# Kernel tuning notes

Measured on AMD Instinct MI355X. Metric: run time of the kernel, lower is better.

## Reference

```python
import jax, jax.numpy as jnp
import numpy as np

B, S, E = 2, 2048, 1024
H = 16
D = E // H  # 64
SCALE = D ** -0.5


def setup_inputs() -> dict:
    key = jax.random.key(0)
    ks = jax.random.split(key, 9)
    w = lambda k: jax.random.normal(k, (E, E), dtype=jnp.float32) * 0.02
    b = lambda k: jax.random.normal(k, (E,), dtype=jnp.float32) * 0.02
    return {
        "hidden_states": jax.random.normal(ks[0], (B, S, E), dtype=jnp.float32),
        "q_w": w(ks[1]), "q_b": b(ks[2]),
        "k_w": w(ks[3]), "k_b": b(ks[4]),
        "v_w": w(ks[5]), "v_b": b(ks[6]),
        "o_w": w(ks[7]), "o_b": b(ks[8]),
    }


def reference(hidden_states, q_w, q_b, k_w, k_b, v_w, v_b, o_w, o_b):
    dtype = hidden_states.dtype
    # torch Linear: y = x @ W^T + b
    q = hidden_states @ q_w.T + q_b
    k = hidden_states @ k_w.T + k_b
    v = hidden_states @ v_w.T + v_b
    # [B,S,E] -> [B*H, S, D]
    split = lambda t: t.reshape(B, S, H, D).transpose(0, 2, 1, 3).reshape(B * H, S, D)
    q, k, v = split(q), split(k), split(v)
    # upcast_attention: fp32 QK^T, scaled (baddbmm with beta=0, no mask)
    scores = SCALE * jnp.einsum("bqd,bkd->bqk", q.astype(jnp.float32), k.astype(jnp.float32))
    # upcast_softmax: fp32 softmax over last dim (transpose_qk=False), cast back
    probs = jax.nn.softmax(scores, axis=-1).astype(dtype)
    # PV bmm, merge heads, out_proj (dropout p=0.0 -> identity)
    out = jnp.einsum("bqk,bkd->bqd", probs, v)
    out = out.reshape(B, H, S, D).transpose(0, 2, 1, 3).reshape(B, S, E)
    return out @ o_w.T + o_b
```

## Files before the change

kernel.cpp:

```cpp
#include <hip/hip_runtime.h>

typedef __bf16 bf16x8 __attribute__((ext_vector_type(8)));
typedef __bf16 bf16x4 __attribute__((ext_vector_type(4)));
typedef float  f32x4  __attribute__((ext_vector_type(4)));
typedef float  f32x16 __attribute__((ext_vector_type(16)));
typedef unsigned int u32x4 __attribute__((ext_vector_type(4)));

#define CS 0.18033688011112042f

__device__ __forceinline__ float fast_exp2(float x) {
    return __builtin_amdgcn_exp2f(x);
}

__device__ __forceinline__ f32x4 MFMA(bf16x8 a, bf16x8 b, f32x4 c) {
    return __builtin_amdgcn_mfma_f32_16x16x32_bf16(a, b, c, 0, 0, 0);
}
__device__ __forceinline__ f32x16 MFMA32(bf16x8 a, bf16x8 b, f32x16 c) {
    return __builtin_amdgcn_mfma_f32_32x32x16_bf16(a, b, c, 0, 0, 0);
}

__device__ __forceinline__ unsigned pk2(float a, float b) {
    union { __bf16 h[2]; unsigned u; } x;
    x.h[0] = (__bf16)a; x.h[1] = (__bf16)b;
    return x.u;
}

__device__ __forceinline__ void swap32(unsigned &a, unsigned &b) {
    asm volatile("v_permlane32_swap_b32 %0, %1" : "+v"(a), "+v"(b));
}

__global__ __launch_bounds__(256) void cvt5_kernel(
    const float* __restrict__ s0, const float* __restrict__ s1,
    const float* __restrict__ s2, const float* __restrict__ s3,
    const float* __restrict__ s4,
    __bf16* __restrict__ d0, __bf16* __restrict__ d1, __bf16* __restrict__ d2,
    __bf16* __restrict__ d3, __bf16* __restrict__ d4)
{
    int blk = blockIdx.x;
    const float* src; __bf16* dst; int base;
    if (blk < 4096)      { src = s0; dst = d0; base = blk; }
    else if (blk < 5120) { src = s1; dst = d1; base = blk - 4096; }
    else if (blk < 6144) { src = s2; dst = d2; base = blk - 5120; }
    else if (blk < 7168) { src = s3; dst = d3; base = blk - 6144; }
    else                 { src = s4; dst = d4; base = blk - 7168; }
    int i = base * 1024 + threadIdx.x * 4;
    float4 v = *(const float4*)(src + i);
    bf16x4 o;
    o[0] = (__bf16)v.x; o[1] = (__bf16)v.y; o[2] = (__bf16)v.z; o[3] = (__bf16)v.w;
    *(bf16x4*)(dst + i) = o;
}

template <typename OutT, int BN>
__device__ __forceinline__ void gemm_core(const __bf16* __restrict__ A,
                                          const __bf16* __restrict__ W,
                                          const float* __restrict__ bias,
                                          OutT* __restrict__ C,
                                          int m0, int n0, bool vtrans, float oscale)
{
    constexpr int NJ = BN / 32;
    __shared__ __bf16 As[128 * 64];
    __shared__ __bf16 Bs[BN * 64];

    const int tid  = threadIdx.x;
    const int lane = tid & 63;
    const int w    = tid >> 6;
    const int wm   = w & 1;
    const int wn   = w >> 1;
    const int s    = lane & 15;
    const int q    = lane >> 4;

    f32x4 acc[4][NJ];
#pragma unroll
    for (int i = 0; i < 4; i++)
#pragma unroll
        for (int j = 0; j < NJ; j++)
#pragma unroll
            for (int r = 0; r < 4; r++) acc[i][j][r] = 0.0f;

    bf16x8 apre[4], bpre[NJ];
#pragma unroll
    for (int t = 0; t < 4; t++) {
        int c = tid + 256 * t, row = c >> 3, cc = c & 7;
        apre[t] = *(const bf16x8*)(A + (size_t)(m0 + row) * 1024 + cc * 8);
    }
#pragma unroll
    for (int t = 0; t < NJ; t++) {
        int c = tid + 256 * t, row = c >> 3, cc = c & 7;
        bpre[t] = *(const bf16x8*)(W + (size_t)(n0 + row) * 1024 + cc * 8);
    }

    for (int k0 = 0; k0 < 1024; k0 += 64) {
        __syncthreads();
#pragma unroll
        for (int t = 0; t < 4; t++) {
            int c = tid + 256 * t, row = c >> 3, cc = c & 7;
            *(bf16x8*)&As[row * 64 + ((cc ^ (row & 7)) << 3)] = apre[t];
        }
#pragma unroll
        for (int t = 0; t < NJ; t++) {
            int c = tid + 256 * t, row = c >> 3, cc = c & 7;
            *(bf16x8*)&Bs[row * 64 + ((cc ^ (row & 7)) << 3)] = bpre[t];
        }
        __syncthreads();

        if (k0 < 1024 - 64) {
            int kn = k0 + 64;
#pragma unroll
            for (int t = 0; t < 4; t++) {
                int c = tid + 256 * t, row = c >> 3, cc = c & 7;
                apre[t] = *(const bf16x8*)(A + (size_t)(m0 + row) * 1024 + kn + cc * 8);
            }
#pragma unroll
            for (int t = 0; t < NJ; t++) {
                int c = tid + 256 * t, row = c >> 3, cc = c & 7;
                bpre[t] = *(const bf16x8*)(W + (size_t)(n0 + row) * 1024 + kn + cc * 8);
            }
        }

#pragma unroll
        for (int kk = 0; kk < 2; kk++) {
            bf16x8 af[4], bf[NJ];
#pragma unroll
            for (int i = 0; i < 4; i++) {
                int row = wm * 64 + i * 16 + s;
                int idx = row * 64 + ((((kk << 2) + q) ^ (row & 7)) << 3);
                af[i] = *(const bf16x8*)&As[idx];
            }
#pragma unroll
            for (int j = 0; j < NJ; j++) {
                int row = wn * (BN / 2) + j * 16 + s;
                int idx = row * 64 + ((((kk << 2) + q) ^ (row & 7)) << 3);
                bf[j] = *(const bf16x8*)&Bs[idx];
            }
#pragma unroll
            for (int i = 0; i < 4; i++)
#pragma unroll
                for (int j = 0; j < NJ; j++)
                    acc[i][j] = MFMA(af[i], bf[j], acc[i][j]);
        }
    }

    if (vtrans) {
        __bf16* Vt = (__bf16*)C;
#pragma unroll
        for (int j = 0; j < NJ; j++) {
            int col = n0 + wn * (BN / 2) + j * 16 + s;
            int h   = col >> 6;
            int d   = col & 63;
            float bv = bias[col];
#pragma unroll
            for (int i = 0; i < 4; i++) {
                int rowb = m0 + wm * 64 + i * 16 + q * 4;
                int b    = rowb >> 11;
                int srow = rowb & 2047;
                bf16x4 pk;
#pragma unroll
                for (int r = 0; r < 4; r++) pk[r] = (__bf16)(acc[i][j][r] + bv);
                *(bf16x4*)&Vt[(size_t)((b * 16 + h) * 64 + d) * 2048 + srow] = pk;
            }
        }
    } else {
#pragma unroll
        for (int j = 0; j < NJ; j++) {
            int col = n0 + wn * (BN / 2) + j * 16 + s;
            float bv = bias[col];
#pragma unroll
            for (int i = 0; i < 4; i++) {
                int rowb = m0 + wm * 64 + i * 16 + q * 4;
#pragma unroll
                for (int r = 0; r < 4; r++) {
                    C[(size_t)(rowb + r) * 1024 + col] = (OutT)((acc[i][j][r] + bv) * oscale);
                }
            }
        }
    }
}

__global__ __launch_bounds__(256) void gemm_qkv_kernel(
    const __bf16* __restrict__ X,
    const __bf16* __restrict__ Wq, const float* __restrict__ bq,
    const __bf16* __restrict__ Wk, const float* __restrict__ bk,
    const __bf16* __restrict__ Wv, const float* __restrict__ bv,
    __bf16* __restrict__ Q, __bf16* __restrict__ K, __bf16* __restrict__ Vt)
{
    int mt   = blockIdx.x & 31;
    int ntot = blockIdx.x >> 5;
    int which = ntot >> 3;
    const __bf16* W    = (which == 0) ? Wq : (which == 1) ? Wk : Wv;
    const float*  bias = (which == 0) ? bq : (which == 1) ? bk : bv;
    __bf16*       Out  = (which == 0) ? Q  : (which == 1) ? K  : Vt;
    float oscale = (which == 0) ? CS : 1.0f;
    gemm_core<__bf16, 128>(X, W, bias, Out, mt * 128, (ntot & 7) * 128, which == 2, oscale);
}

__global__ __launch_bounds__(256) void gemm_o_kernel(
    const __bf16* __restrict__ Ain, const __bf16* __restrict__ Wo,
    const float* __restrict__ bo, float* __restrict__ Out)
{
    int mt = blockIdx.x & 31;
    int nt = blockIdx.x >> 5;
    gemm_core<float, 64>(Ain, Wo, bo, Out, mt * 128, nt * 64, false, 1.0f);
}

__global__ __launch_bounds__(512, 4) void attn_kernel(
    const __bf16* __restrict__ Q, const __bf16* __restrict__ K,
    const __bf16* __restrict__ Vt, __bf16* __restrict__ O)
{
    __shared__ __bf16 smem[2][2][2][64 * 64];

    const int bh = blockIdx.x >> 4;
    const int qt = blockIdx.x & 15;
    const int b  = bh >> 4;
    const int h  = bh & 15;

    const int tid  = threadIdx.x;
    const int lane = tid & 63;
    const int w    = tid >> 6;
    const int g    = w >> 2;
    const int ws   = w & 3;
    const int lt   = tid & 255;
    const int qc   = lane & 31;
    const int hi   = lane >> 5;

    bf16x8 bq[4];
    {
        const int qrow = qt * 128 + ws * 32 + qc;
        const __bf16* qp = Q + (size_t)(b * 2048 + qrow) * 1024 + h * 64 + hi * 8;
#pragma unroll
        for (int kd = 0; kd < 4; kd++)
            bq[kd] = *(const bf16x8*)(qp + kd * 16);
    }

    f32x16 acc[2];
#pragma unroll
    for (int nb = 0; nb < 2; nb++)
#pragma unroll
        for (int r = 0; r < 16; r++) acc[nb][r] = 0.0f;
    float lst = 0.0f;

    const __bf16* Kbase = K  + (size_t)(b * 2048 + g * 1024) * 1024 + h * 64;
    const __bf16* Vbase = Vt + (size_t)bh * 64 * 2048 + g * 1024;

    bf16x8 kpre[2], vpre[2];
#pragma unroll
    for (int t = 0; t < 2; t++) {
        int c = lt + 256 * t;
        int krow = c >> 3, s16 = c & 7;
        kpre[t] = *(const bf16x8*)(Kbase + (size_t)krow * 1024 + s16 * 8);
        vpre[t] = *(const bf16x8*)(Vbase + (size_t)krow * 2048 + s16 * 8);
    }
#pragma unroll
    for (int t = 0; t < 2; t++) {
        int c = lt + 256 * t;
        int krow = c >> 3, s16 = c & 7;
        *(bf16x8*)&smem[g][0][0][krow * 64 + ((s16 ^ (krow & 7)) << 3)] = kpre[t];
        *(bf16x8*)&smem[g][0][1][krow * 64 + ((s16 ^ (krow & 7)) << 3)] = vpre[t];
    }
#pragma unroll
    for (int t = 0; t < 2; t++) {
        int c = lt + 256 * t;
        int krow = c >> 3, s16 = c & 7;
        kpre[t] = *(const bf16x8*)(Kbase + (size_t)(64 + krow) * 1024 + s16 * 8);
        vpre[t] = *(const bf16x8*)(Vbase + (size_t)krow * 2048 + 64 + s16 * 8);
    }
    __syncthreads();

    int cur = 0;
    for (int kc = 0; kc < 16; kc++) {
        {
            __bf16* kwb = smem[g][cur ^ 1][0];
            __bf16* vwb = smem[g][cur ^ 1][1];
#pragma unroll
            for (int t = 0; t < 2; t++) {
                int c = lt + 256 * t;
                int krow = c >> 3, s16 = c & 7;
                *(bf16x8*)&kwb[krow * 64 + ((s16 ^ (krow & 7)) << 3)] = kpre[t];
                *(bf16x8*)&vwb[krow * 64 + ((s16 ^ (krow & 7)) << 3)] = vpre[t];
            }
        }
        {
            int kb2 = ((kc + 2) & 15) * 64;
#pragma unroll
            for (int t = 0; t < 2; t++) {
                int c = lt + 256 * t;
                int krow = c >> 3, s16 = c & 7;
                kpre[t] = *(const bf16x8*)(Kbase + (size_t)(kb2 + krow) * 1024 + s16 * 8);
                vpre[t] = *(const bf16x8*)(Vbase + (size_t)krow * 2048 + kb2 + s16 * 8);
            }
        }

        const __bf16* kbuf = smem[g][cur][0];
        const __bf16* vbuf = smem[g][cur][1];

        f32x16 sc[2];
#pragma unroll
        for (int mb = 0; mb < 2; mb++)
#pragma unroll
            for (int r = 0; r < 16; r++) sc[mb][r] = 0.0f;
#pragma unroll
        for (int mb = 0; mb < 2; mb++) {
            int row = mb * 32 + qc;
            int rsw = row & 7;
#pragma unroll
            for (int kd = 0; kd < 4; kd++) {
                bf16x8 af = *(const bf16x8*)&kbuf[row * 64 + ((((kd << 1) | hi) ^ rsw) << 3)];
                sc[mb] = MFMA32(af, bq[kd], sc[mb]);
            }
        }

#pragma unroll
        for (int mb = 0; mb < 2; mb++) {
            float e[16];
#pragma unroll
            for (int r = 0; r < 16; r++)
                e[r] = fast_exp2(sc[mb][r]);
            float s0 = 0.f, s1 = 0.f, s2 = 0.f, s3 = 0.f;
#pragma unroll
            for (int r = 0; r < 16; r += 4) {
                s0 += e[r]; s1 += e[r + 1]; s2 += e[r + 2]; s3 += e[r + 3];
            }
            lst += (s0 + s1) + (s2 + s3);
#pragma unroll
            for (int bb = 0; bb < 2; bb++) {
                unsigned w0 = pk2(e[8 * bb + 0], e[8 * bb + 1]);
                unsigned w1 = pk2(e[8 * bb + 2], e[8 * bb + 3]);
                unsigned w2 = pk2(e[8 * bb + 4], e[8 * bb + 5]);
                unsigned w3 = pk2(e[8 * bb + 6], e[8 * bb + 7]);
                swap32(w0, w2);
                swap32(w1, w3);
                u32x4 pw; pw[0] = w0; pw[1] = w1; pw[2] = w2; pw[3] = w3;
                bf16x8 pa = __builtin_bit_cast(bf16x8, pw);
                int kslot = ((mb << 1) | bb) << 1;
#pragma unroll
                for (int nb = 0; nb < 2; nb++) {
                    int d = nb * 32 + qc;
                    bf16x8 bv = *(const bf16x8*)&vbuf[d * 64 + (((kslot | hi) ^ (d & 7)) << 3)];
                    acc[nb] = MFMA32(pa, bv, acc[nb]);
                }
            }
        }
        __syncthreads();
        cur ^= 1;
    }

    float* cbuf = (float*)&smem[0][0][0][0];
    if (g == 1) {
        float* p = cbuf + ((size_t)ws * 64 + lane) * 36;
        *(f32x16*)(p)      = acc[0];
        *(f32x16*)(p + 16) = acc[1];
        p[32] = lst;
    }
    __syncthreads();
    if (g == 0) {
        float* p = cbuf + ((size_t)ws * 64 + lane) * 36;
        acc[0] += *(const f32x16*)(p);
        acc[1] += *(const f32x16*)(p + 16);
        lst += p[32];

        float lt2 = lst + __shfl_xor(lst, 32);

        const size_t obase = (size_t)(b * 2048 + qt * 128 + ws * 32) * 1024 + h * 64;
#pragma unroll
        for (int r = 0; r < 16; r++) {
            int row_rel = (r & 3) + 8 * (r >> 2) + 4 * hi;
            float lr = __shfl(lt2, row_rel);
            float inv = 1.0f / lr;
#pragma unroll
            for (int nb = 0; nb < 2; nb++) {
                O[obase + (size_t)row_rel * 1024 + nb * 32 + qc] = (__bf16)(acc[nb][r] * inv);
            }
        }
    }
}

extern "C" void kernel_launch(void* const* d_in, const int* in_sizes, int n_in,
                              void* d_out, int out_size, void* d_ws, size_t ws_size,
                              hipStream_t stream)
{
    const float* hs = (const float*)d_in[0];
    const float* qw = (const float*)d_in[1];
    const float* qb = (const float*)d_in[2];
    const float* kw = (const float*)d_in[3];
    const float* kb = (const float*)d_in[4];
    const float* vw = (const float*)d_in[5];
    const float* vb = (const float*)d_in[6];
    const float* ow = (const float*)d_in[7];
    const float* ob = (const float*)d_in[8];
    float* out = (float*)d_out;

    char* ws = (char*)d_ws;
    const size_t MB = (size_t)1024 * 1024;
    __bf16* Xb  = (__bf16*)(ws);
    __bf16* Wqb = (__bf16*)(ws +  8 * MB);
    __bf16* Wkb = (__bf16*)(ws + 10 * MB);
    __bf16* Wvb = (__bf16*)(ws + 12 * MB);
    __bf16* Wob = (__bf16*)(ws + 14 * MB);
    __bf16* Qb  = (__bf16*)(ws + 16 * MB);
    __bf16* Kb  = (__bf16*)(ws + 24 * MB);
    __bf16* Vtb = (__bf16*)(ws + 32 * MB);
    __bf16* Ab  = (__bf16*)(ws + 40 * MB);

    cvt5_kernel<<<dim3(8192), dim3(256), 0, stream>>>(hs, qw, kw, vw, ow,
                                                      Xb, Wqb, Wkb, Wvb, Wob);

    gemm_qkv_kernel<<<dim3(768), dim3(256), 0, stream>>>(Xb, Wqb, qb, Wkb, kb, Wvb, vb,
                                                         Qb, Kb, Vtb);
    attn_kernel<<<dim3(512), dim3(512), 0, stream>>>(Qb, Kb, Vtb, Ab);
    gemm_o_kernel<<<dim3(512), dim3(256), 0, stream>>>(Ab, Wob, ob, out);
}
```

Measured before the change: 193.6 us.

## Load GEMM tiles via global_load_lds and raise priority around attention MFMAs

The projection GEMM stops staging tiles through registers and instead uses direct global-to-LDS 16-byte loads. The software prefetch and the XOR swizzle are dropped, so the tiles are now stored unswizzled in LDS. In the attention kernel, the MFMA calls are wrapped in s_setprio to favour matrix issue, and the score accumulator is initialised by the first MFMA. The GEMM loses its overlap of the next tile's global loads with compute and may now see LDS bank conflicts, in exchange for lower VGPR use and fewer instructions.

```diff
diff --git a/kernel.cpp b/kernel.cpp
--- a/kernel.cpp
+++ b/kernel.cpp
@@ -10,6 +10,12 @@
 
 __device__ __forceinline__ float fast_exp2(float x) {
     return __builtin_amdgcn_exp2f(x);
+}
+
+__device__ __forceinline__ void gload_lds16(const __bf16* g, __bf16* l) {
+    __builtin_amdgcn_global_load_lds(
+        (const __attribute__((address_space(1))) void*)g,
+        (__attribute__((address_space(3))) void*)l, 16, 0, 0);
 }
 
 __device__ __forceinline__ f32x4 MFMA(bf16x8 a, bf16x8 b, f32x4 c) {
@@ -57,7 +63,8 @@
                                           OutT* __restrict__ C,
                                           int m0, int n0, bool vtrans, float oscale)
 {
-    constexpr int NJ = BN / 32;
+    constexpr int NJ  = BN / 32;
+    constexpr int BCH = BN / 32;
     __shared__ __bf16 As[128 * 64];
     __shared__ __bf16 Bs[BN * 64];
 
@@ -69,6 +76,9 @@
     const int s    = lane & 15;
     const int q    = lane >> 4;
 
+    const int srow = lane >> 3;
+    const int scol = lane & 7;
+
     f32x4 acc[4][NJ];
 #pragma unroll
     for (int i = 0; i < 4; i++)
@@ -76,46 +86,24 @@
         for (int j = 0; j < NJ; j++)
 #pragma unroll
             for (int r = 0; r < 4; r++) acc[i][j][r] = 0.0f;
-
-    bf16x8 apre[4], bpre[NJ];
-#pragma unroll
-    for (int t = 0; t < 4; t++) {
-        int c = tid + 256 * t, row = c >> 3, cc = c & 7;
-        apre[t] = *(const bf16x8*)(A + (size_t)(m0 + row) * 1024 + cc * 8);
-    }
-#pragma unroll
-    for (int t = 0; t < NJ; t++) {
-        int c = tid + 256 * t, row = c >> 3, cc = c & 7;
-        bpre[t] = *(const bf16x8*)(W + (size_t)(n0 + row) * 1024 + cc * 8);
-    }
 
     for (int k0 = 0; k0 < 1024; k0 += 64) {
         __syncthreads();
 #pragma unroll
         for (int t = 0; t < 4; t++) {
-            int c = tid + 256 * t, row = c >> 3, cc = c & 7;
-            *(bf16x8*)&As[row * 64 + ((cc ^ (row & 7)) << 3)] = apre[t];
-        }
-#pragma unroll
-        for (int t = 0; t < NJ; t++) {
-            int c = tid + 256 * t, row = c >> 3, cc = c & 7;
-            *(bf16x8*)&Bs[row * 64 + ((cc ^ (row & 7)) << 3)] = bpre[t];
+            int chunk = w * 4 + t;
+            int row   = chunk * 8 + srow;
+            gload_lds16(A + (size_t)(m0 + row) * 1024 + k0 + scol * 8,
+                        &As[chunk * 512]);
+        }
+#pragma unroll
+        for (int t = 0; t < BCH; t++) {
+            int chunk = w * BCH + t;
+            int row   = chunk * 8 + srow;
+            gload_lds16(W + (size_t)(n0 + row) * 1024 + k0 + scol * 8,
+                        &Bs[chunk * 512]);
         }
         __syncthreads();
-
-        if (k0 < 1024 - 64) {
-            int kn = k0 + 64;
-#pragma unroll
-            for (int t = 0; t < 4; t++) {
-                int c = tid + 256 * t, row = c >> 3, cc = c & 7;
-                apre[t] = *(const bf16x8*)(A + (size_t)(m0 + row) * 1024 + kn + cc * 8);
-            }
-#pragma unroll
-            for (int t = 0; t < NJ; t++) {
-                int c = tid + 256 * t, row = c >> 3, cc = c & 7;
-                bpre[t] = *(const bf16x8*)(W + (size_t)(n0 + row) * 1024 + kn + cc * 8);
-            }
-        }
 
 #pragma unroll
         for (int kk = 0; kk < 2; kk++) {
@@ -123,14 +111,12 @@
 #pragma unroll
             for (int i = 0; i < 4; i++) {
                 int row = wm * 64 + i * 16 + s;
-                int idx = row * 64 + ((((kk << 2) + q) ^ (row & 7)) << 3);
-                af[i] = *(const bf16x8*)&As[idx];
+                af[i] = *(const bf16x8*)&As[row * 64 + ((kk << 2) + q) * 8];
             }
 #pragma unroll
             for (int j = 0; j < NJ; j++) {
                 int row = wn * (BN / 2) + j * 16 + s;
-                int idx = row * 64 + ((((kk << 2) + q) ^ (row & 7)) << 3);
-                bf[j] = *(const bf16x8*)&Bs[idx];
+                bf[j] = *(const bf16x8*)&Bs[row * 64 + ((kk << 2) + q) * 8];
             }
 #pragma unroll
             for (int i = 0; i < 4; i++)
@@ -152,11 +138,11 @@
             for (int i = 0; i < 4; i++) {
                 int rowb = m0 + wm * 64 + i * 16 + q * 4;
                 int b    = rowb >> 11;
-                int srow = rowb & 2047;
+                int sr   = rowb & 2047;
                 bf16x4 pk;
 #pragma unroll
                 for (int r = 0; r < 4; r++) pk[r] = (__bf16)(acc[i][j][r] + bv);
-                *(bf16x4*)&Vt[(size_t)((b * 16 + h) * 64 + d) * 2048 + srow] = pk;
+                *(bf16x4*)&Vt[(size_t)((b * 16 + h) * 64 + d) * 2048 + sr] = pk;
             }
         }
     } else {
@@ -231,11 +217,10 @@
             bq[kd] = *(const bf16x8*)(qp + kd * 16);
     }
 
+    const f32x16 fzero = 0.0f;
     f32x16 acc[2];
 #pragma unroll
-    for (int nb = 0; nb < 2; nb++)
-#pragma unroll
-        for (int r = 0; r < 16; r++) acc[nb][r] = 0.0f;
+    for (int nb = 0; nb < 2; nb++) acc[nb] = fzero;
     float lst = 0.0f;
 
     const __bf16* Kbase = K  + (size_t)(b * 2048 + g * 1024) * 1024 + h * 64;
@@ -294,17 +279,19 @@
 
         f32x16 sc[2];
 #pragma unroll
-        for (int mb = 0; mb < 2; mb++)
-#pragma unroll
-            for (int r = 0; r < 16; r++) sc[mb][r] = 0.0f;
-#pragma unroll
         for (int mb = 0; mb < 2; mb++) {
             int row = mb * 32 + qc;
             int rsw = row & 7;
-#pragma unroll
-            for (int kd = 0; kd < 4; kd++) {
+            bf16x8 af0 = *(const bf16x8*)&kbuf[row * 64 + ((hi ^ rsw) << 3)];
+            __builtin_amdgcn_s_setprio(1);
+            sc[mb] = MFMA32(af0, bq[0], fzero);
+            __builtin_amdgcn_s_setprio(0);
+#pragma unroll
+            for (int kd = 1; kd < 4; kd++) {
                 bf16x8 af = *(const bf16x8*)&kbuf[row * 64 + ((((kd << 1) | hi) ^ rsw) << 3)];
+                __builtin_amdgcn_s_setprio(1);
                 sc[mb] = MFMA32(af, bq[kd], sc[mb]);
+                __builtin_amdgcn_s_setprio(0);
             }
         }
 
@@ -331,12 +318,12 @@
                 u32x4 pw; pw[0] = w0; pw[1] = w1; pw[2] = w2; pw[3] = w3;
                 bf16x8 pa = __builtin_bit_cast(bf16x8, pw);
                 int kslot = ((mb << 1) | bb) << 1;
-#pragma unroll
-                for (int nb = 0; nb < 2; nb++) {
-                    int d = nb * 32 + qc;
-                    bf16x8 bv = *(const bf16x8*)&vbuf[d * 64 + (((kslot | hi) ^ (d & 7)) << 3)];
-                    acc[nb] = MFMA32(pa, bv, acc[nb]);
-                }
+                bf16x8 bv0 = *(const bf16x8*)&vbuf[(0 * 32 + qc) * 64 + (((kslot | hi) ^ (qc & 7)) << 3)];
+                bf16x8 bv1 = *(const bf16x8*)&vbuf[(1 * 32 + qc) * 64 + (((kslot | hi) ^ ((32 + qc) & 7)) << 3)];
+                __builtin_amdgcn_s_setprio(1);
+                acc[0] = MFMA32(pa, bv0, acc[0]);
+                acc[1] = MFMA32(pa, bv1, acc[1]);
+                __builtin_amdgcn_s_setprio(0);
             }
         }
         __syncthreads();
```

Result: slower. 205.6 us (+6.2%).
